# Optimization experiments

Measured on AMD Instinct MI355X. Metric: run time of the kernel, lower is better.

Reference implementation:

```python
import jax, jax.numpy as jnp
import numpy as np

SEQ, B, D_IN, D_H = 512, 64, 512, 512


def setup_inputs() -> dict:
    key = jax.random.key(0)
    ks = jax.random.split(key, 5)
    s = 1.0 / np.sqrt(D_IN + D_H)
    inp = {
        "inputs": jax.random.normal(ks[0], (SEQ, B, D_IN), dtype=jnp.float32),
        "W_f": jax.random.normal(ks[1], (D_H, D_IN + D_H), dtype=jnp.float32) * s,
        "b_f": jnp.zeros((D_H,), jnp.float32),
        "W_i": jax.random.normal(ks[2], (D_H, D_IN + D_H), dtype=jnp.float32) * s,
        "b_i": jnp.zeros((D_H,), jnp.float32),
        "W_g": jax.random.normal(ks[3], (D_H, D_IN + D_H), dtype=jnp.float32) * s,
        "b_g": jnp.zeros((D_H,), jnp.float32),
        "W_o": jax.random.normal(ks[4], (D_H, D_IN + D_H), dtype=jnp.float32) * s,
        "b_o": jnp.zeros((D_H,), jnp.float32),
    }
    return inp


def reference(inputs, W_f, b_f, W_i, b_i, W_g, b_g, W_o, b_o):
    # inputs: [seq, batch, d_in]; states start at zeros (module default)
    B_ = inputs.shape[1]
    h0 = jnp.zeros((B_, D_H), inputs.dtype)
    c0 = jnp.zeros((B_, D_H), inputs.dtype)

    def step(carry, x_t):
        hx, cx = carry
        combined = jnp.concatenate([x_t, hx], axis=1)  # [B, d_in+d_h]
        f = jax.nn.sigmoid(combined @ W_f.T + b_f)
        i = jax.nn.sigmoid(combined @ W_i.T + b_i)
        g = jnp.tanh(combined @ W_g.T + b_g)
        o = jax.nn.sigmoid(combined @ W_o.T + b_o)
        cx = f * cx + i * g
        hx = o * jnp.tanh(cx)
        return (hx, cx), hx

    (hx, cx), stacked = jax.lax.scan(step, (h0, c0), inputs)
    return stacked, hx, cx
```

## Files before the change

### kernel.cpp

```cpp
#include <hip/hip_runtime.h>

#define SEQ   512
#define BATCH 64
#define DIN   512
#define DH    512
#define KTOT  1024
#define NWG   128
#define NTH   256
#define HBUF_BYTES 65536

#define FLAGS_BYTES 65536
#define HBASE_OFF   65536
#define XBF_OFF     (HBASE_OFF + 512 * HBUF_BYTES)
#define XBF_BYTES   ((size_t)SEQ * 4 * 16 * 1024)
#define WS_MODE1    ((size_t)HBASE_OFF + 511 * HBUF_BYTES)
#define WS_MODE2    ((size_t)XBF_OFF + XBF_BYTES)
#define FLAG_STRIDE 32

typedef __attribute__((ext_vector_type(8))) short short8;
typedef __attribute__((ext_vector_type(4))) float f32x4;

__device__ __forceinline__ float sig_(float v) { return 1.0f / (1.0f + __expf(-v)); }
__device__ __forceinline__ float tanh_fast(float v) {
    const float e = __expf(2.0f * v);
    return 1.0f - 2.0f / (e + 1.0f);
}

__device__ __forceinline__ unsigned int f2bf(float f) {
    unsigned int u = __float_as_uint(f);
    return (u + 0x7fffu + ((u >> 16) & 1u)) >> 16;
}

__device__ __forceinline__ short8 cvt8(float4 lo, float4 hi) {
    short8 r;
    r[0] = (short)f2bf(lo.x); r[1] = (short)f2bf(lo.y);
    r[2] = (short)f2bf(lo.z); r[3] = (short)f2bf(lo.w);
    r[4] = (short)f2bf(hi.x); r[5] = (short)f2bf(hi.y);
    r[6] = (short)f2bf(hi.z); r[7] = (short)f2bf(hi.w);
    return r;
}

__device__ __forceinline__ unsigned int ld_flag(const unsigned int* p) {
    return __hip_atomic_load(p, __ATOMIC_RELAXED, __HIP_MEMORY_SCOPE_AGENT);
}
__device__ __forceinline__ void st_flag(unsigned int* p, unsigned int v) {
    __hip_atomic_store(p, v, __ATOMIC_RELAXED, __HIP_MEMORY_SCOPE_AGENT);
}
__device__ __forceinline__ unsigned long long ld_h_sc1(const unsigned long long* p) {
    return __hip_atomic_load(p, __ATOMIC_RELAXED, __HIP_MEMORY_SCOPE_AGENT);
}
__device__ __forceinline__ void st_h(unsigned long long* p, unsigned long long v) {
    __hip_atomic_store(p, v, __ATOMIC_RELAXED, __HIP_MEMORY_SCOPE_AGENT);
}

__global__ __launch_bounds__(256)
void xconv(const float* __restrict__ x, unsigned short* __restrict__ xbf)
{
    const int gid = blockIdx.x * 256 + threadIdx.x;
    const int l   = gid & 63;
    const int kt  = (gid >> 6) & 15;
    const int mtt = (gid >> 10) & 3;
    const int t   = gid >> 12;
    const float* src = x + ((size_t)t * BATCH + mtt * 16 + (l & 15)) * DIN
                         + kt * 32 + (l >> 4) * 8;
    *(short8*)(xbf + (size_t)gid * 8) =
        cvt8(*(const float4*)src, *(const float4*)(src + 4));
}

template <int MODE>
__global__ __launch_bounds__(NTH, 1)
void lstm_mfma(const float* __restrict__ x,
               const unsigned short* __restrict__ xbf,
               const float* __restrict__ Wf, const float* __restrict__ bfp,
               const float* __restrict__ Wi, const float* __restrict__ bip,
               const float* __restrict__ Wg, const float* __restrict__ bgp,
               const float* __restrict__ Wo, const float* __restrict__ bop,
               float* __restrict__ out,
               unsigned int* __restrict__ ws_u32)
{
    const int tid = threadIdx.x;
    const int l   = tid & 63;
    const int mt  = tid >> 6;
    const int wg  = blockIdx.x;
    const int j0  = wg * 4;

    const int n    = l & 15;
    const int khi  = l >> 4;

    unsigned int* const flags = ws_u32;
    char* const hbase = (char*)ws_u32 + HBASE_OFF;

    const float* Wn = (n < 8) ? ((n < 4) ? Wf : Wi) : ((n < 12) ? Wg : Wo);
    const float* wrow = Wn + (size_t)(j0 + (n & 3)) * KTOT + khi * 8;
    short8 Bfr[32];
    #pragma unroll
    for (int kt = 0; kt < 32; ++kt) {
        Bfr[kt] = cvt8(*(const float4*)(wrow + kt * 32),
                       *(const float4*)(wrow + kt * 32 + 4));
    }
    const float biasn = ((n < 8) ? ((n < 4) ? bfp : bip)
                                 : ((n < 12) ? bgp : bop))[j0 + (n & 3)];

    float cst0 = 0.f, cst1 = 0.f, cst2 = 0.f, cst3 = 0.f;

    float* const hx_out = out + (size_t)SEQ * BATCH * DH;
    float* const cx_out = hx_out + (size_t)BATCH * DH;

    const int kth         = wg >> 3;
    const int lane_f_base = ((wg & 7) >> 1) << 4;
    const int half8       = (wg & 1) * 8;

    const unsigned int* const f0p = flags + ((size_t)mt * 128 + l) * FLAG_STRIDE;
    const unsigned int* const f1p = f0p + (size_t)64 * FLAG_STRIDE;
    unsigned int* const my_flag = flags + ((size_t)mt * 128 + wg) * FLAG_STRIDE;

    const float*  xrow_base = x + (size_t)(mt * 16 + (l & 15)) * DIN + khi * 8;
    const short8* xbf_base  = (const short8*)xbf + (size_t)mt * 16 * 64 + l;

    for (int t = 0; t < SEQ; ++t) {
        f32x4 acc = {0.f, 0.f, 0.f, 0.f};

        if (MODE == 2) {
            const short8* xp = xbf_base + (size_t)t * 4096;
            #pragma unroll
            for (int kt = 0; kt < 16; ++kt) {
                acc = __builtin_amdgcn_mfma_f32_16x16x32_bf16(xp[kt * 64], Bfr[kt],
                                                              acc, 0, 0, 0);
            }
        } else {
            const float* xr = xrow_base + (size_t)t * BATCH * DIN;
            #pragma unroll
            for (int kt = 0; kt < 16; ++kt) {
                const short8 a = cvt8(*(const float4*)(xr + kt * 32),
                                      *(const float4*)(xr + kt * 32 + 4));
                acc = __builtin_amdgcn_mfma_f32_16x16x32_bf16(a, Bfr[kt], acc, 0, 0, 0);
            }
        }

        if (t > 0) {
            const unsigned int target = (unsigned int)t;
            for (;;) {
                const unsigned int fa = ld_flag(f0p);
                const unsigned int fb = ld_flag(f1p);
                if (__all(fa >= target && fb >= target)) break;
                __builtin_amdgcn_s_sleep(1);
            }
            asm volatile("" ::: "memory");

            if (MODE == 0) {
                const unsigned long long* hp =
                    (const unsigned long long*)(hbase + ((t & 1) ^ 1) * HBUF_BYTES)
                    + ((size_t)(mt * 16) * 64 + l) * 2;
                #pragma unroll
                for (int kt = 0; kt < 16; ++kt) {
                    union { unsigned long long u[2]; short8 v; } U;
                    U.u[0] = ld_h_sc1(hp + kt * 128);
                    U.u[1] = ld_h_sc1(hp + kt * 128 + 1);
                    acc = __builtin_amdgcn_mfma_f32_16x16x32_bf16(U.v, Bfr[16 + kt],
                                                                  acc, 0, 0, 0);
                }
            } else {
                const uint4* hp = (const uint4*)(hbase + (size_t)(t - 1) * HBUF_BYTES)
                                  + ((size_t)(mt * 16) * 64 + l);
                uint4 hv[16];
                #pragma unroll
                for (int kt = 0; kt < 16; ++kt) hv[kt] = hp[kt * 64];
                #pragma unroll
                for (int kt = 0; kt < 16; ++kt) {
                    union { uint4 u; short8 v; } U; U.u = hv[kt];
                    acc = __builtin_amdgcn_mfma_f32_16x16x32_bf16(U.v, Bfr[16 + kt],
                                                                  acc, 0, 0, 0);
                }
            }
        }

        const float p0 = acc[0] + biasn;
        const float p1 = acc[1] + biasn;
        const float p2 = acc[2] + biasn;
        const float p3 = acc[3] + biasn;

        const float i0 = __shfl_xor(p0, 4), g0 = __shfl_xor(p0, 8), o0 = __shfl_xor(p0, 12);
        const float i1 = __shfl_xor(p1, 4), g1 = __shfl_xor(p1, 8), o1 = __shfl_xor(p1, 12);
        const float i2 = __shfl_xor(p2, 4), g2 = __shfl_xor(p2, 8), o2 = __shfl_xor(p2, 12);
        const float i3 = __shfl_xor(p3, 4), g3 = __shfl_xor(p3, 8), o3 = __shfl_xor(p3, 12);

        const bool active = ((l >> 2) & 3) == 0;
        float v0 = 0.f, v1 = 0.f, v2 = 0.f, v3 = 0.f;
        int   bT = 0;

        if (active) {
            float hq0, hq1, hq2, hq3;
            cst0 = fmaf(sig_(p0), cst0, sig_(i0) * tanh_fast(g0)); hq0 = sig_(o0) * tanh_fast(cst0);
            cst1 = fmaf(sig_(p1), cst1, sig_(i1) * tanh_fast(g1)); hq1 = sig_(o1) * tanh_fast(cst1);
            cst2 = fmaf(sig_(p2), cst2, sig_(i2) * tanh_fast(g2)); hq2 = sig_(o2) * tanh_fast(cst2);
            cst3 = fmaf(sig_(p3), cst3, sig_(i3) * tanh_fast(g3)); hq3 = sig_(o3) * tanh_fast(cst3);

            const int src = l & 48;
            const int jc  = l & 3;
            #pragma unroll
            for (int q = 0; q < 4; ++q) {
                const float hqq = (q == 0) ? hq0 : (q == 1) ? hq1 : (q == 2) ? hq2 : hq3;
                #pragma unroll
                for (int jj = 0; jj < 4; ++jj) {
                    const float tsh = __shfl(hqq, src + jj);
                    if (jc == q) {
                        if (jj == 0) v0 = tsh; else if (jj == 1) v1 = tsh;
                        else if (jj == 2) v2 = tsh; else v3 = tsh;
                    }
                }
            }
            bT = mt * 16 + ((l >> 4) << 2) + jc;

            if (t < SEQ - 1) {
                const unsigned long long pk =
                    (unsigned long long)(f2bf(v0) | (f2bf(v1) << 16))
                    | ((unsigned long long)(f2bf(v2) | (f2bf(v3) << 16)) << 32);
                char* const wb = (MODE == 0) ? hbase + (t & 1) * HBUF_BYTES
                                             : hbase + (size_t)t * HBUF_BYTES;
                unsigned long long* hp_w = (unsigned long long*)
                    (wb + (((size_t)(mt * 16 + kth) * 64
                            + (lane_f_base | (bT & 15))) << 4) + half8);
                st_h(hp_w, pk);
            }
        }

        if (t < SEQ - 1) {
            asm volatile("s_waitcnt vmcnt(0)" ::: "memory");
            if (l == 0) st_flag(my_flag, (unsigned int)(t + 1));
        }

        if (active) {
            const float4 ov = make_float4(v0, v1, v2, v3);
            *(float4*)(out + ((size_t)t * BATCH + bT) * DH + j0) = ov;
            if (t == SEQ - 1) {
                *(float4*)(hx_out + (size_t)bT * DH + j0) = ov;
                const int b0 = mt * 16 + ((l >> 4) << 2);
                const int j  = j0 + (l & 3);
                cx_out[(size_t)b0 * DH + j]       = cst0;
                cx_out[(size_t)(b0 + 1) * DH + j] = cst1;
                cx_out[(size_t)(b0 + 2) * DH + j] = cst2;
                cx_out[(size_t)(b0 + 3) * DH + j] = cst3;
            }
        }
    }
}

extern "C" void kernel_launch(void* const* d_in, const int* in_sizes, int n_in,
                              void* d_out, int out_size, void* d_ws, size_t ws_size,
                              hipStream_t stream)
{
    const float* x  = (const float*)d_in[0];
    const float* Wf = (const float*)d_in[1];
    const float* bf = (const float*)d_in[2];
    const float* Wi = (const float*)d_in[3];
    const float* bi = (const float*)d_in[4];
    const float* Wg = (const float*)d_in[5];
    const float* bg = (const float*)d_in[6];
    const float* Wo = (const float*)d_in[7];
    const float* bo = (const float*)d_in[8];
    float* out = (float*)d_out;

    hipMemsetAsync(d_ws, 0, FLAGS_BYTES, stream);

    unsigned int* wsp = (unsigned int*)d_ws;
    if (ws_size >= WS_MODE2) {
        unsigned short* xbf = (unsigned short*)((char*)d_ws + XBF_OFF);
        xconv<<<SEQ * 4 * 16 * 64 / 256, 256, 0, stream>>>(x, xbf);
        lstm_mfma<2><<<NWG, NTH, 0, stream>>>(x, xbf, Wf, bf, Wi, bi,
                                              Wg, bg, Wo, bo, out, wsp);
    } else if (ws_size >= WS_MODE1) {
        lstm_mfma<1><<<NWG, NTH, 0, stream>>>(x, nullptr, Wf, bf, Wi, bi,
                                              Wg, bg, Wo, bo, out, wsp);
    } else {
        lstm_mfma<0><<<NWG, NTH, 0, stream>>>(x, nullptr, Wf, bf, Wi, bi,
                                              Wg, bg, Wo, bo, out, wsp);
    }
}
```

Measured before the change: 2.461 ms.

## Use one flag per workgroup with block barrier; compute gate activations before shuffle

```diff
diff --git a/kernel.cpp b/kernel.cpp
--- a/kernel.cpp
+++ b/kernel.cpp
@@ -20,7 +20,6 @@
 typedef __attribute__((ext_vector_type(8))) short short8;
 typedef __attribute__((ext_vector_type(4))) float f32x4;
 
-__device__ __forceinline__ float sig_(float v) { return 1.0f / (1.0f + __expf(-v)); }
 __device__ __forceinline__ float tanh_fast(float v) {
     const float e = __expf(2.0f * v);
     return 1.0f - 2.0f / (e + 1.0f);
@@ -86,6 +85,7 @@
 
     const int n    = l & 15;
     const int khi  = l >> 4;
+    const bool isg = ((n >> 2) == 2);
 
     unsigned int* const flags = ws_u32;
     char* const hbase = (char*)ws_u32 + HBASE_OFF;
@@ -110,9 +110,9 @@
     const int lane_f_base = ((wg & 7) >> 1) << 4;
     const int half8       = (wg & 1) * 8;
 
-    const unsigned int* const f0p = flags + ((size_t)mt * 128 + l) * FLAG_STRIDE;
+    const unsigned int* const f0p = flags + (size_t)l * FLAG_STRIDE;
     const unsigned int* const f1p = f0p + (size_t)64 * FLAG_STRIDE;
-    unsigned int* const my_flag = flags + ((size_t)mt * 128 + wg) * FLAG_STRIDE;
+    unsigned int* const my_flag = flags + (size_t)wg * FLAG_STRIDE;
 
     const float*  xrow_base = x + (size_t)(mt * 16 + (l & 15)) * DIN + khi * 8;
     const short8* xbf_base  = (const short8*)xbf + (size_t)mt * 16 * 64 + l;
@@ -138,14 +138,17 @@
         }
 
         if (t > 0) {
-            const unsigned int target = (unsigned int)t;
-            for (;;) {
-                const unsigned int fa = ld_flag(f0p);
-                const unsigned int fb = ld_flag(f1p);
-                if (__all(fa >= target && fb >= target)) break;
-                __builtin_amdgcn_s_sleep(1);
-            }
-            asm volatile("" ::: "memory");
+            if (mt == 0) {
+                const unsigned int target = (unsigned int)t;
+                for (;;) {
+                    const unsigned int fa = ld_flag(f0p);
+                    const unsigned int fb = ld_flag(f1p);
+                    if (__all(fa >= target && fb >= target)) break;
+                    __builtin_amdgcn_s_sleep(1);
+                }
+                asm volatile("" ::: "memory");
+            }
+            __syncthreads();
 
             if (MODE == 0) {
                 const unsigned long long* hp =
@@ -174,15 +177,22 @@
             }
         }
 
-        const float p0 = acc[0] + biasn;
-        const float p1 = acc[1] + biasn;
-        const float p2 = acc[2] + biasn;
-        const float p3 = acc[3] + biasn;
-
-        const float i0 = __shfl_xor(p0, 4), g0 = __shfl_xor(p0, 8), o0 = __shfl_xor(p0, 12);
-        const float i1 = __shfl_xor(p1, 4), g1 = __shfl_xor(p1, 8), o1 = __shfl_xor(p1, 12);
-        const float i2 = __shfl_xor(p2, 4), g2 = __shfl_xor(p2, 8), o2 = __shfl_xor(p2, 12);
-        const float i3 = __shfl_xor(p3, 4), g3 = __shfl_xor(p3, 8), o3 = __shfl_xor(p3, 12);
+        float aq0, aq1, aq2, aq3;
+        {
+            const float m = isg ? 2.0f : 1.0f;
+            const float y0 = 1.0f / (1.0f + __expf(-m * (acc[0] + biasn)));
+            const float y1 = 1.0f / (1.0f + __expf(-m * (acc[1] + biasn)));
+            const float y2 = 1.0f / (1.0f + __expf(-m * (acc[2] + biasn)));
+            const float y3 = 1.0f / (1.0f + __expf(-m * (acc[3] + biasn)));
+            aq0 = isg ? 2.0f * y0 - 1.0f : y0;
+            aq1 = isg ? 2.0f * y1 - 1.0f : y1;
+            aq2 = isg ? 2.0f * y2 - 1.0f : y2;
+            aq3 = isg ? 2.0f * y3 - 1.0f : y3;
+        }
+        const float i0 = __shfl_xor(aq0, 4), g0 = __shfl_xor(aq0, 8), o0 = __shfl_xor(aq0, 12);
+        const float i1 = __shfl_xor(aq1, 4), g1 = __shfl_xor(aq1, 8), o1 = __shfl_xor(aq1, 12);
+        const float i2 = __shfl_xor(aq2, 4), g2 = __shfl_xor(aq2, 8), o2 = __shfl_xor(aq2, 12);
+        const float i3 = __shfl_xor(aq3, 4), g3 = __shfl_xor(aq3, 8), o3 = __shfl_xor(aq3, 12);
 
         const bool active = ((l >> 2) & 3) == 0;
         float v0 = 0.f, v1 = 0.f, v2 = 0.f, v3 = 0.f;
@@ -190,10 +200,10 @@
 
         if (active) {
             float hq0, hq1, hq2, hq3;
-            cst0 = fmaf(sig_(p0), cst0, sig_(i0) * tanh_fast(g0)); hq0 = sig_(o0) * tanh_fast(cst0);
-            cst1 = fmaf(sig_(p1), cst1, sig_(i1) * tanh_fast(g1)); hq1 = sig_(o1) * tanh_fast(cst1);
-            cst2 = fmaf(sig_(p2), cst2, sig_(i2) * tanh_fast(g2)); hq2 = sig_(o2) * tanh_fast(cst2);
-            cst3 = fmaf(sig_(p3), cst3, sig_(i3) * tanh_fast(g3)); hq3 = sig_(o3) * tanh_fast(cst3);
+            cst0 = fmaf(aq0, cst0, i0 * g0); hq0 = o0 * tanh_fast(cst0);
+            cst1 = fmaf(aq1, cst1, i1 * g1); hq1 = o1 * tanh_fast(cst1);
+            cst2 = fmaf(aq2, cst2, i2 * g2); hq2 = o2 * tanh_fast(cst2);
+            cst3 = fmaf(aq3, cst3, i3 * g3); hq3 = o3 * tanh_fast(cst3);
 
             const int src = l & 48;
             const int jc  = l & 3;
@@ -226,7 +236,8 @@
 
         if (t < SEQ - 1) {
             asm volatile("s_waitcnt vmcnt(0)" ::: "memory");
-            if (l == 0) st_flag(my_flag, (unsigned int)(t + 1));
+            __syncthreads();
+            if (tid == 0) st_flag(my_flag, (unsigned int)(t + 1));
         }
 
         if (active) {
```

After: 2.329 ms. -5.3%, faster.
